# Performance work log

Measured on AMD Instinct MI355X. Metric: run time of the kernel, lower is better.

## Reference

```python
import jax, jax.numpy as jnp
import numpy as np

B, S, H = 1, 2048, 1024
NH, NKV, HD = 16, 4, 64  # n_attn_heads, n_kv_heads, head_dim


def setup_inputs() -> dict:
    key = jax.random.key(0)
    k1, k2, k3, k4 = jax.random.split(key, 4)
    x = jax.random.normal(k1, (B, S, H), dtype=jnp.float32)
    Wq = jax.random.normal(k2, (H, H), dtype=jnp.float32) * 0.02
    Wk = jax.random.normal(k3, (NKV * HD, H), dtype=jnp.float32) * 0.02
    Wv = jax.random.normal(k4, (NKV * HD, H), dtype=jnp.float32) * 0.02
    return {"x": x, "Wq": Wq, "Wk": Wk, "Wv": Wv}


def reference(x, Wq, Wk, Wv):
    b, s, h = x.shape
    rep = NH // NKV
    # projections (torch Linear: x @ W.T)
    q = (x @ Wq.T).reshape(b, s, NH, HD).transpose(0, 2, 1, 3)      # [b, NH, s, d]
    k = (x @ Wk.T).reshape(b, s, NKV, HD).transpose(0, 2, 1, 3)     # [b, NKV, s, d]
    v = (x @ Wv.T).reshape(b, s, NKV, HD).transpose(0, 2, 1, 3)
    # repeat_kv: expand each kv head rep times
    k = jnp.repeat(k, rep, axis=1)                                   # [b, NH, s, d]
    v = jnp.repeat(v, rep, axis=1)
    # NOTE: source scales by 1/sqrt(hidden_size), not 1/sqrt(head_dim)
    scale = 1.0 / np.sqrt(H).astype(np.float32)
    scores = jnp.einsum('bhqd,bhkd->bhqk', q, k) * scale             # [b, NH, s, s]
    causal = jnp.tril(jnp.ones((s, s), dtype=bool))
    scores = jnp.where(causal[None, None], scores, -jnp.inf)
    probs = jax.nn.softmax(scores, axis=-1)
    y = jnp.einsum('bhqk,bhkd->bhqd', probs, v)                      # [b, NH, s, d]
    return y.transpose(0, 2, 1, 3).reshape(b, s, NH * HD)
```

## Files before the change

### kernel.cpp

```cpp
#include <hip/hip_runtime.h>

#define S_LEN 2048
#define HID   1024
#define NHEAD 16
#define NKVH  4
#define HDIM  64
#define NPROJ 1536
#define QKSTR 1280

typedef __bf16 bf16x8 __attribute__((ext_vector_type(8)));
typedef float  f32x4  __attribute__((ext_vector_type(4)));

typedef const __attribute__((address_space(1))) void* gas_ptr;
typedef __attribute__((address_space(3))) void*       las_ptr;

#define QSCALE 0.04508422f

__device__ __forceinline__ unsigned short f2bf(float f) {
    unsigned u = __builtin_bit_cast(unsigned, f);
    u = u + 0x7FFFu + ((u >> 16) & 1u);
    return (unsigned short)(u >> 16);
}

__global__ __launch_bounds__(256) void cvt_all(
    const float* __restrict__ x,  const float* __restrict__ wq,
    const float* __restrict__ wk, const float* __restrict__ wv,
    unsigned short* __restrict__ xbf, unsigned short* __restrict__ wbf)
{
    const long nx  = (long)S_LEN * HID;
    const long nwq = (long)HID * HID;
    const long nwk = (long)256 * HID;
    long i = (long)(blockIdx.x * 256 + threadIdx.x) * 4;
    const float* src; unsigned short* dst;
    if (i < nx)                  { src = x  + i;                 dst = xbf + i; }
    else if (i < nx + nwq)       { long j = i - nx;              src = wq + j; dst = wbf + j; }
    else if (i < nx + nwq + nwk) { long j = i - nx - nwq;        src = wk + j; dst = wbf + nwq + j; }
    else                         { long j = i - nx - nwq - nwk;  src = wv + j; dst = wbf + nwq + nwk + j; }
    float4 v = *(const float4*)src;
    ushort4 o; o.x = f2bf(v.x); o.y = f2bf(v.y); o.z = f2bf(v.z); o.w = f2bf(v.w);
    *(ushort4*)dst = o;
}

__global__ __launch_bounds__(256) void proj_gemm(
    const unsigned short* __restrict__ xbf,
    const unsigned short* __restrict__ wbf,
    unsigned short* __restrict__ qkv,
    unsigned short* __restrict__ vT)
{
    __shared__ unsigned short At[2][128 * 64];
    __shared__ unsigned short Bt[2][96 * 64];
    const int tid = threadIdx.x;
    const int w = tid >> 6, l = tid & 63;
    const int quad = l >> 4, lane16 = l & 15;
    const int m0 = blockIdx.y * 128, n0 = blockIdx.x * 96;
    const int wm = (w & 1) * 64, wn = (w >> 1) * 48;

    const int srow = l >> 3;
    const int scol = ((l & 7) ^ srow) * 8;

    f32x4 acc[4][3] = {};

    #define STAGE(KT, BUF)                                                              \
        do {                                                                            \
            _Pragma("unroll")                                                           \
            for (int c = 0; c < 4; ++c) {                                               \
                const int rbase = w * 32 + c * 8;                                       \
                const unsigned short* ga =                                              \
                    xbf + (long)(m0 + rbase + srow) * HID + (KT) + scol;                \
                __builtin_amdgcn_global_load_lds((gas_ptr)ga,                           \
                    (las_ptr)&At[BUF][rbase * 64], 16, 0, 0);                           \
            }                                                                           \
            _Pragma("unroll")                                                           \
            for (int c = 0; c < 3; ++c) {                                               \
                const int rbase = w * 24 + c * 8;                                       \
                const unsigned short* gb =                                              \
                    wbf + (long)(n0 + rbase + srow) * HID + (KT) + scol;                \
                __builtin_amdgcn_global_load_lds((gas_ptr)gb,                           \
                    (las_ptr)&Bt[BUF][rbase * 64], 16, 0, 0);                           \
            }                                                                           \
        } while (0)

    STAGE(0, 0);

    for (int i = 0; i < 16; ++i) {
        const int cur = i & 1;
        __syncthreads();
        if (i + 1 < 16) STAGE((i + 1) * 64, cur ^ 1);

        #pragma unroll
        for (int ks = 0; ks < 2; ++ks) {
            const int swz = ((ks * 4 + quad) ^ (lane16 & 7)) * 8;
            bf16x8 a[4], b[3];
            #pragma unroll
            for (int mi = 0; mi < 4; ++mi)
                a[mi] = *(const bf16x8*)&At[cur][(wm + mi * 16 + lane16) * 64 + swz];
            #pragma unroll
            for (int ni = 0; ni < 3; ++ni)
                b[ni] = *(const bf16x8*)&Bt[cur][(wn + ni * 16 + lane16) * 64 + swz];
            #pragma unroll
            for (int mi = 0; mi < 4; ++mi)
                #pragma unroll
                for (int ni = 0; ni < 3; ++ni)
                    acc[mi][ni] = __builtin_amdgcn_mfma_f32_16x16x32_bf16(a[mi], b[ni], acc[mi][ni], 0, 0, 0);
        }
    }
    #undef STAGE

    #pragma unroll
    for (int mi = 0; mi < 4; ++mi) {
        const int row = m0 + wm + mi * 16 + quad * 4;
        #pragma unroll
        for (int ni = 0; ni < 3; ++ni) {
            const int col = n0 + wn + ni * 16 + lane16;
            #pragma unroll
            for (int r = 0; r < 4; ++r) {
                const float v = acc[mi][ni][r];
                if (col < 1024)
                    qkv[(long)(row + r) * QKSTR + col] = f2bf(v * QSCALE);
                else if (col < 1280)
                    qkv[(long)(row + r) * QKSTR + col] = f2bf(v);
                else
                    vT[(long)(col - 1280) * S_LEN + (row + r)] = f2bf(v);
            }
        }
    }
}

#define KSTR 72
__global__ __launch_bounds__(256) void attn(
    const unsigned short* __restrict__ qkv,
    const unsigned short* __restrict__ vT,
    float* __restrict__ out)
{
    __shared__ unsigned short Kt[2][64 * KSTR];
    __shared__ unsigned short Vt[2][64 * KSTR];
    __shared__ unsigned short Pb[4 * 16 * KSTR];

    const int tid = threadIdx.x;
    const int w = tid >> 6, l = tid & 63;
    const int quad = l >> 4, lane16 = l & 15;
    const int bx = blockIdx.x, by = blockIdx.y;
    const int qt = (by & 8) ? (31 - bx) : bx;
    const int h  = by;
    const int kh = h >> 2;
    const int qcol = h * 64;
    const int kcol = 1024 + kh * 64;

    const long qrow = (long)(qt * 64 + w * 16 + lane16);
    bf16x8 qa0 = *(const bf16x8*)&qkv[qrow * QKSTR + qcol + quad * 8];
    bf16x8 qa1 = *(const bf16x8*)&qkv[qrow * QKSTR + qcol + 32 + quad * 8];

    f32x4 o[4] = {};
    float rsum[4] = {0.f, 0.f, 0.f, 0.f};

    unsigned short* pw = &Pb[w * 16 * KSTR];

    const int sr = tid >> 2, ss = tid & 3;
    const long vrow = (long)(kh * 64 + sr) * S_LEN;

    bf16x8 kr0, kr1, vr0, vr1;
    {
        const long gk = (long)sr * QKSTR + kcol + ss * 16;
        kr0 = *(const bf16x8*)&qkv[gk];
        kr1 = *(const bf16x8*)&qkv[gk + 8];
        const long gv = vrow + ss * 16;
        vr0 = *(const bf16x8*)&vT[gv];
        vr1 = *(const bf16x8*)&vT[gv + 8];
    }

    for (int kt = 0; kt <= qt; ++kt) {
        const int cur = kt & 1;
        *(bf16x8*)&Kt[cur][sr * KSTR + ss * 16]     = kr0;
        *(bf16x8*)&Kt[cur][sr * KSTR + ss * 16 + 8] = kr1;
        *(bf16x8*)&Vt[cur][sr * KSTR + ss * 16]     = vr0;
        *(bf16x8*)&Vt[cur][sr * KSTR + ss * 16 + 8] = vr1;
        if (kt < qt) {
            const long gk = (long)((kt + 1) * 64 + sr) * QKSTR + kcol + ss * 16;
            kr0 = *(const bf16x8*)&qkv[gk];
            kr1 = *(const bf16x8*)&qkv[gk + 8];
            const long gv = vrow + (kt + 1) * 64 + ss * 16;
            vr0 = *(const bf16x8*)&vT[gv];
            vr1 = *(const bf16x8*)&vT[gv + 8];
        }
        __syncthreads();

        f32x4 sacc[4] = {};
        #pragma unroll
        for (int t = 0; t < 4; ++t) {
            bf16x8 kb0 = *(const bf16x8*)&Kt[cur][(t * 16 + lane16) * KSTR + quad * 8];
            bf16x8 kb1 = *(const bf16x8*)&Kt[cur][(t * 16 + lane16) * KSTR + 32 + quad * 8];
            sacc[t] = __builtin_amdgcn_mfma_f32_16x16x32_bf16(qa0, kb0, sacc[t], 0, 0, 0);
            sacc[t] = __builtin_amdgcn_mfma_f32_16x16x32_bf16(qa1, kb1, sacc[t], 0, 0, 0);
        }

        if (kt == qt) {
            #pragma unroll
            for (int t = 0; t < 4; ++t) {
                const int colw = t * 16 + lane16;
                #pragma unroll
                for (int r = 0; r < 4; ++r)
                    if (colw > w * 16 + quad * 4 + r) sacc[t][r] = -3.0e38f;
            }
        }

        #pragma unroll
        for (int t = 0; t < 4; ++t)
            #pragma unroll
            for (int r = 0; r < 4; ++r) {
                const float p = __builtin_amdgcn_exp2f(sacc[t][r]);
                rsum[r] += p;
                const int row = quad * 4 + r;
                const int col = t * 16 + lane16;
                pw[row * KSTR + (col ^ ((row & 12) << 1))] = f2bf(p);
            }

        __syncthreads();

        #pragma unroll
        for (int ks = 0; ks < 2; ++ks) {
            bf16x8 pa = *(const bf16x8*)&pw[lane16 * KSTR + ((ks * 32 + quad * 8) ^ ((lane16 & 12) << 1))];
            #pragma unroll
            for (int t = 0; t < 4; ++t) {
                bf16x8 vb = *(const bf16x8*)&Vt[cur][(t * 16 + lane16) * KSTR + ks * 32 + quad * 8];
                o[t] = __builtin_amdgcn_mfma_f32_16x16x32_bf16(pa, vb, o[t], 0, 0, 0);
            }
        }
    }

    float inv[4];
    #pragma unroll
    for (int r = 0; r < 4; ++r) {
        float v = rsum[r];
        v += __shfl_xor(v, 1);
        v += __shfl_xor(v, 2);
        v += __shfl_xor(v, 4);
        v += __shfl_xor(v, 8);
        inv[r] = 1.0f / v;
    }
    const int orow = qt * 64 + w * 16 + quad * 4;
    #pragma unroll
    for (int t = 0; t < 4; ++t) {
        const int col = h * 64 + t * 16 + lane16;
        #pragma unroll
        for (int r = 0; r < 4; ++r)
            out[(long)(orow + r) * (NHEAD * HDIM) + col] = o[t][r] * inv[r];
    }
}

extern "C" void kernel_launch(void* const* d_in, const int* in_sizes, int n_in,
                              void* d_out, int out_size, void* d_ws, size_t ws_size,
                              hipStream_t stream) {
    const float* x  = (const float*)d_in[0];
    const float* wq = (const float*)d_in[1];
    const float* wk = (const float*)d_in[2];
    const float* wv = (const float*)d_in[3];
    float* out = (float*)d_out;

    unsigned short* xbf = (unsigned short*)d_ws;
    unsigned short* wbf = xbf + (size_t)S_LEN * HID;
    unsigned short* qkv = wbf + (size_t)NPROJ * HID;
    unsigned short* vT  = qkv + (size_t)S_LEN * QKSTR;

    cvt_all<<<dim3(3584), dim3(256), 0, stream>>>(x, wq, wk, wv, xbf, wbf);
    proj_gemm<<<dim3(16, 16), dim3(256), 0, stream>>>(xbf, wbf, qkv, vT);
    attn<<<dim3(32, 16), dim3(256), 0, stream>>>(qkv, vT, out);
}
```

Before: 124.1 us.

## Split causal attention KV range into chunks with separate reduction kernel

Attention work for each query tile is split into up to four KV chunks of eight tiles, giving 80 blocks per head instead of 32 and balancing the causal triangle. Each chunk writes unnormalized partial outputs and row sums to workspace, and a new reduce kernel sums them and normalizes. K/V shared buffers drop from double to single buffering, and the sync moves to the top of the loop. This adds an extra launch and global round-trip for partials. Summing partials directly without max rescaling is only valid because the softmax skips the running max.

```diff
diff --git a/kernel.cpp b/kernel.cpp
--- a/kernel.cpp
+++ b/kernel.cpp
@@ -7,6 +7,7 @@
 #define HDIM  64
 #define NPROJ 1536
 #define QKSTR 1280
+#define PCHUNK 4160
 
 typedef __bf16 bf16x8 __attribute__((ext_vector_type(8)));
 typedef float  f32x4  __attribute__((ext_vector_type(4)));
@@ -127,21 +128,28 @@
 }
 
 #define KSTR 72
-__global__ __launch_bounds__(256) void attn(
+__global__ __launch_bounds__(256) void attn_part(
     const unsigned short* __restrict__ qkv,
     const unsigned short* __restrict__ vT,
-    float* __restrict__ out)
+    float* __restrict__ part)
 {
-    __shared__ unsigned short Kt[2][64 * KSTR];
-    __shared__ unsigned short Vt[2][64 * KSTR];
+    __shared__ unsigned short Kt[64 * KSTR];
+    __shared__ unsigned short Vt[64 * KSTR];
     __shared__ unsigned short Pb[4 * 16 * KSTR];
 
     const int tid = threadIdx.x;
     const int w = tid >> 6, l = tid & 63;
     const int quad = l >> 4, lane16 = l & 15;
-    const int bx = blockIdx.x, by = blockIdx.y;
-    const int qt = (by & 8) ? (31 - bx) : bx;
-    const int h  = by;
+    const int c = blockIdx.x, h = blockIdx.y;
+
+    int qt, ch;
+    if (c < 8)       { qt = c;              ch = 0;            }
+    else if (c < 24) { qt = 8 + (c - 8) / 2;  ch = (c - 8) % 2;  }
+    else if (c < 48) { qt = 16 + (c - 24) / 3; ch = (c - 24) % 3; }
+    else             { qt = 24 + (c - 48) / 4; ch = (c - 48) % 4; }
+    const int kv0 = ch * 8;
+    const int kv1 = min(kv0 + 8, qt + 1);
+
     const int kh = h >> 2;
     const int qcol = h * 64;
     const int kcol = 1024 + kh * 64;
@@ -160,21 +168,21 @@
 
     bf16x8 kr0, kr1, vr0, vr1;
     {
-        const long gk = (long)sr * QKSTR + kcol + ss * 16;
+        const long gk = (long)(kv0 * 64 + sr) * QKSTR + kcol + ss * 16;
         kr0 = *(const bf16x8*)&qkv[gk];
         kr1 = *(const bf16x8*)&qkv[gk + 8];
-        const long gv = vrow + ss * 16;
+        const long gv = vrow + kv0 * 64 + ss * 16;
         vr0 = *(const bf16x8*)&vT[gv];
         vr1 = *(const bf16x8*)&vT[gv + 8];
     }
 
-    for (int kt = 0; kt <= qt; ++kt) {
-        const int cur = kt & 1;
-        *(bf16x8*)&Kt[cur][sr * KSTR + ss * 16]     = kr0;
-        *(bf16x8*)&Kt[cur][sr * KSTR + ss * 16 + 8] = kr1;
-        *(bf16x8*)&Vt[cur][sr * KSTR + ss * 16]     = vr0;
-        *(bf16x8*)&Vt[cur][sr * KSTR + ss * 16 + 8] = vr1;
-        if (kt < qt) {
+    for (int kt = kv0; kt < kv1; ++kt) {
+        __syncthreads();
+        *(bf16x8*)&Kt[sr * KSTR + ss * 16]     = kr0;
+        *(bf16x8*)&Kt[sr * KSTR + ss * 16 + 8] = kr1;
+        *(bf16x8*)&Vt[sr * KSTR + ss * 16]     = vr0;
+        *(bf16x8*)&Vt[sr * KSTR + ss * 16 + 8] = vr1;
+        if (kt + 1 < kv1) {
             const long gk = (long)((kt + 1) * 64 + sr) * QKSTR + kcol + ss * 16;
             kr0 = *(const bf16x8*)&qkv[gk];
             kr1 = *(const bf16x8*)&qkv[gk + 8];
@@ -187,8 +195,8 @@
         f32x4 sacc[4] = {};
         #pragma unroll
         for (int t = 0; t < 4; ++t) {
-            bf16x8 kb0 = *(const bf16x8*)&Kt[cur][(t * 16 + lane16) * KSTR + quad * 8];
-            bf16x8 kb1 = *(const bf16x8*)&Kt[cur][(t * 16 + lane16) * KSTR + 32 + quad * 8];
+            bf16x8 kb0 = *(const bf16x8*)&Kt[(t * 16 + lane16) * KSTR + quad * 8];
+            bf16x8 kb1 = *(const bf16x8*)&Kt[(t * 16 + lane16) * KSTR + 32 + quad * 8];
             sacc[t] = __builtin_amdgcn_mfma_f32_16x16x32_bf16(qa0, kb0, sacc[t], 0, 0, 0);
             sacc[t] = __builtin_amdgcn_mfma_f32_16x16x32_bf16(qa1, kb1, sacc[t], 0, 0, 0);
         }
@@ -214,20 +222,27 @@
                 pw[row * KSTR + (col ^ ((row & 12) << 1))] = f2bf(p);
             }
 
-        __syncthreads();
 
         #pragma unroll
         for (int ks = 0; ks < 2; ++ks) {
             bf16x8 pa = *(const bf16x8*)&pw[lane16 * KSTR + ((ks * 32 + quad * 8) ^ ((lane16 & 12) << 1))];
             #pragma unroll
             for (int t = 0; t < 4; ++t) {
-                bf16x8 vb = *(const bf16x8*)&Vt[cur][(t * 16 + lane16) * KSTR + ks * 32 + quad * 8];
+                bf16x8 vb = *(const bf16x8*)&Vt[(t * 16 + lane16) * KSTR + ks * 32 + quad * 8];
                 o[t] = __builtin_amdgcn_mfma_f32_16x16x32_bf16(pa, vb, o[t], 0, 0, 0);
             }
         }
     }
 
-    float inv[4];
+    float* pb = part + ((long)((h * 32 + qt) * 4 + ch)) * PCHUNK;
+    const int rl = w * 16 + quad * 4;
+    #pragma unroll
+    for (int t = 0; t < 4; ++t) {
+        const int col = t * 16 + lane16;
+        #pragma unroll
+        for (int r = 0; r < 4; ++r)
+            pb[(rl + r) * 64 + col] = o[t][r];
+    }
     #pragma unroll
     for (int r = 0; r < 4; ++r) {
         float v = rsum[r];
@@ -235,15 +250,39 @@
         v += __shfl_xor(v, 2);
         v += __shfl_xor(v, 4);
         v += __shfl_xor(v, 8);
-        inv[r] = 1.0f / v;
-    }
-    const int orow = qt * 64 + w * 16 + quad * 4;
+        if (lane16 == 0) pb[4096 + rl + r] = v;
+    }
+}
+
+__global__ __launch_bounds__(256) void attn_reduce(
+    const float* __restrict__ part, float* __restrict__ out)
+{
+    const int qt = blockIdx.x, h = blockIdx.y;
+    const int nch = (qt < 8) ? 1 : (qt < 16) ? 2 : (qt < 24) ? 3 : 4;
+    const float* pb = part + ((long)(h * 32 + qt) * 4) * PCHUNK;
+
+    const int tid = threadIdx.x;
+    const int row = tid >> 2, colb = (tid & 3) * 16;
+
+    float lsum = 0.0f;
+    for (int cc = 0; cc < nch; ++cc) lsum += pb[cc * PCHUNK + 4096 + row];
+    const float inv = 1.0f / lsum;
+
+    float4 acc[4] = {};
+    for (int cc = 0; cc < nch; ++cc) {
+        const float* src = &pb[cc * PCHUNK + row * 64 + colb];
+        #pragma unroll
+        for (int j = 0; j < 4; ++j) {
+            float4 v = *(const float4*)&src[j * 4];
+            acc[j].x += v.x; acc[j].y += v.y; acc[j].z += v.z; acc[j].w += v.w;
+        }
+    }
+    float* dst = &out[(long)(qt * 64 + row) * (NHEAD * HDIM) + h * 64 + colb];
     #pragma unroll
-    for (int t = 0; t < 4; ++t) {
-        const int col = h * 64 + t * 16 + lane16;
-        #pragma unroll
-        for (int r = 0; r < 4; ++r)
-            out[(long)(orow + r) * (NHEAD * HDIM) + col] = o[t][r] * inv[r];
+    for (int j = 0; j < 4; ++j) {
+        float4 v; v.x = acc[j].x * inv; v.y = acc[j].y * inv;
+        v.z = acc[j].z * inv; v.w = acc[j].w * inv;
+        *(float4*)&dst[j * 4] = v;
     }
 }
 
@@ -260,8 +299,10 @@
     unsigned short* wbf = xbf + (size_t)S_LEN * HID;
     unsigned short* qkv = wbf + (size_t)NPROJ * HID;
     unsigned short* vT  = qkv + (size_t)S_LEN * QKSTR;
+    float* part = (float*)(vT + (size_t)256 * S_LEN);
 
     cvt_all<<<dim3(3584), dim3(256), 0, stream>>>(x, wq, wk, wv, xbf, wbf);
     proj_gemm<<<dim3(16, 16), dim3(256), 0, stream>>>(xbf, wbf, qkv, vT);
-    attn<<<dim3(32, 16), dim3(256), 0, stream>>>(qkv, vT, out);
-}
+    attn_part<<<dim3(80, 16), dim3(256), 0, stream>>>(qkv, vT, part);
+    attn_reduce<<<dim3(32, 16), dim3(256), 0, stream>>>(part, out);
+}
```

After: 128.8 us. 3.7% more time.
